# Optimization experiments

Measured on AMD Instinct MI355X. Metric: run time of the kernel, lower is better.

The kernel has to match this reference:

```python
import jax, jax.numpy as jnp
import numpy as np

B, S, DIM_IN, DIM_K, DIM_V = 8, 4096, 1024, 128, 128


def setup_inputs() -> dict:
    key = jax.random.key(0)
    ks = jax.random.split(key, 9)
    s_in = 1.0 / np.sqrt(DIM_IN)
    return {
        "query": jax.random.normal(ks[0], (B, S, DIM_IN), jnp.float32),
        "key": jax.random.normal(ks[1], (B, S, DIM_IN), jnp.float32),
        "value": jax.random.normal(ks[2], (B, S, DIM_IN), jnp.float32),
        # Linear params stored as [in, out] (torch weight transposed)
        "Wq": jax.random.uniform(ks[3], (DIM_IN, DIM_K), jnp.float32, -s_in, s_in),
        "bq": jax.random.uniform(ks[4], (DIM_K,), jnp.float32, -s_in, s_in),
        "Wk": jax.random.uniform(ks[5], (DIM_IN, DIM_K), jnp.float32, -s_in, s_in),
        "bk": jax.random.uniform(ks[6], (DIM_K,), jnp.float32, -s_in, s_in),
        "Wv": jax.random.uniform(ks[7], (DIM_IN, DIM_V), jnp.float32, -s_in, s_in),
        "bv": jax.random.uniform(ks[8], (DIM_V,), jnp.float32, -s_in, s_in),
    }


def reference(query, key, value, Wq, bq, Wk, bk, Wv, bv):
    q = jnp.einsum("bsd,dk->bsk", query, Wq) + bq   # [B,S,DIM_K]
    k = jnp.einsum("bsd,dk->bsk", key, Wk) + bk     # [B,S,DIM_K]
    v = jnp.einsum("bsd,dv->bsv", value, Wv) + bv   # [B,S,DIM_V]
    scale = 1.0 / jnp.sqrt(jnp.asarray(q.shape[-1], q.dtype))
    scores = jnp.einsum("bqk,bsk->bqs", q, k) * scale  # [B,S,S]
    attn = jax.nn.softmax(scores, axis=-1)
    return jnp.einsum("bqs,bsv->bqv", attn, v)  # [B,S,DIM_V]
```

## Files before the change

kernel.cpp:

```cpp
#include <hip/hip_runtime.h>
#include <hip/hip_bf16.h>

typedef __attribute__((ext_vector_type(8))) short short8;
typedef __attribute__((ext_vector_type(4))) float f32x4;
typedef __attribute__((ext_vector_type(16))) float f32x16;
typedef __attribute__((ext_vector_type(4))) unsigned int u32x4;

#define MFMA32(A, B, C) __builtin_amdgcn_mfma_f32_32x32x16_bf16((A), (B), (C), 0, 0, 0)

__device__ __forceinline__ short f2bf(float x) {
  unsigned u = __float_as_uint(x);
  return (short)((u + 0x7FFFu + ((u >> 16) & 1u)) >> 16);
}

__device__ __forceinline__ unsigned cvtpk(float lo, float hi) {
  unsigned r;
  asm("v_cvt_pk_bf16_f32 %0, %1, %2" : "=v"(r) : "v"(lo), "v"(hi));
  return r;
}

__device__ __forceinline__ void gload16(const void* g, const void* s) {
  __builtin_amdgcn_global_load_lds(
      (const __attribute__((address_space(1))) unsigned int*)g,
      (__attribute__((address_space(3))) unsigned int*)s, 16, 0, 0);
}

__global__ __launch_bounds__(256) void wt_kernel(
    const float* __restrict__ Wq, const float* __restrict__ Wk, const float* __restrict__ Wv,
    short* __restrict__ WqT, short* __restrict__ WkT, short* __restrict__ WvT)
{
  const float* W  = (blockIdx.y == 0) ? Wq  : (blockIdx.y == 1) ? Wk  : Wv;
  short*       WT = (blockIdx.y == 0) ? WqT : (blockIdx.y == 1) ? WkT : WvT;
  int idx = blockIdx.x * 256 + threadIdx.x;
  int n = idx >> 10, k = idx & 1023;
  WT[idx] = f2bf(W[k * 128 + n]);
}

__global__ __launch_bounds__(256, 2) void proj_kernel(
    const float* __restrict__ Aq, const float* __restrict__ Ak, const float* __restrict__ Av,
    const short* __restrict__ WqT, const short* __restrict__ WkT, const short* __restrict__ WvT,
    const float* __restrict__ bq, const float* __restrict__ bk, const float* __restrict__ bv,
    short* __restrict__ Qs, short* __restrict__ Ks, short* __restrict__ VTs,
    float scale_q)
{
  __shared__ short lds[32768];
  const int y = blockIdx.y;
  const float* A    = (y == 0) ? Aq  : (y == 1) ? Ak  : Av;
  const short* WT   = (y == 0) ? WqT : (y == 1) ? WkT : WvT;
  const float* bias = (y == 0) ? bq  : (y == 1) ? bk  : bv;
  const int tid = threadIdx.x, l = tid & 63, w = tid >> 6;
  const int l31 = l & 31, hi = l >> 5;
  const long m0 = (long)blockIdx.x * 128;
  const long mw = m0 + w * 32;

  const float* A0 = A + m0 * 1024;
  int ag[8];
  #pragma unroll
  for (int i = 0; i < 8; ++i) {
    int p = i * 4096 + tid * 16;
    int r_ = p >> 8;
    int c_ = (p & 255) ^ ((r_ & 15) << 4);
    ag[i] = r_ * 1024 + (c_ >> 2);
  }

  #define ASTAGE(bb, kc) { \
    const float* s_ = A0 + (kc) * 64; \
    _Pragma("unroll") \
    for (int i = 0; i < 8; ++i) \
      gload16(s_ + ag[i], &lds[(bb) * 16384 + i * 2048 + w * 512]); \
  }

  f32x16 acc0 = {}, acc1 = {}, acc2 = {}, acc3 = {};
  const char* abase = (const char*)lds;
  const int arow = w * 32 + l31;
  const int sw = (l31 & 15) << 4;
  const short* wl = WT + (long)l31 * 1024 + hi * 8;

  ASTAGE(0, 0);

  for (int kc = 0; kc < 16; ++kc) {
    const int bb = kc & 1;
    if (kc + 1 < 16) {
      ASTAGE(bb ^ 1, kc + 1);
      asm volatile("s_waitcnt vmcnt(8)" ::: "memory");
    } else {
      asm volatile("s_waitcnt vmcnt(0)" ::: "memory");
    }
    __builtin_amdgcn_s_barrier();

    const char* ab = abase + bb * 32768 + arow * 256;
    if (y < 2) {
      #pragma unroll
      for (int ks = 0; ks < 4; ++ks) {
        const int ac = ks * 64 + hi * 32;
        f32x4 a0 = *(const f32x4*)(ab + ((ac)      ^ sw));
        f32x4 a1 = *(const f32x4*)(ab + ((ac + 16) ^ sw));
        short8 af;
        af[0] = f2bf(a0[0]); af[1] = f2bf(a0[1]); af[2] = f2bf(a0[2]); af[3] = f2bf(a0[3]);
        af[4] = f2bf(a1[0]); af[5] = f2bf(a1[1]); af[6] = f2bf(a1[2]); af[7] = f2bf(a1[3]);
        const short* wp = wl + kc * 64 + ks * 16;
        short8 b0 = *(const short8*)(wp);
        short8 b1 = *(const short8*)(wp + 32768);
        short8 b2 = *(const short8*)(wp + 65536);
        short8 b3 = *(const short8*)(wp + 98304);
        acc0 = MFMA32(af, b0, acc0);
        acc1 = MFMA32(af, b1, acc1);
        acc2 = MFMA32(af, b2, acc2);
        acc3 = MFMA32(af, b3, acc3);
      }
    } else {
      #pragma unroll
      for (int ks = 0; ks < 4; ++ks) {
        const int ac = ks * 64 + hi * 32;
        f32x4 a0 = *(const f32x4*)(ab + ((ac)      ^ sw));
        f32x4 a1 = *(const f32x4*)(ab + ((ac + 16) ^ sw));
        short8 af;
        af[0] = f2bf(a0[0]); af[1] = f2bf(a0[1]); af[2] = f2bf(a0[2]); af[3] = f2bf(a0[3]);
        af[4] = f2bf(a1[0]); af[5] = f2bf(a1[1]); af[6] = f2bf(a1[2]); af[7] = f2bf(a1[3]);
        const short* wp = wl + kc * 64 + ks * 16;
        short8 b0 = *(const short8*)(wp);
        short8 b1 = *(const short8*)(wp + 32768);
        short8 b2 = *(const short8*)(wp + 65536);
        short8 b3 = *(const short8*)(wp + 98304);
        acc0 = MFMA32(b0, af, acc0);
        acc1 = MFMA32(b1, af, acc1);
        acc2 = MFMA32(b2, af, acc2);
        acc3 = MFMA32(b3, af, acc3);
      }
    }
    asm volatile("s_waitcnt lgkmcnt(0)" ::: "memory");
    __builtin_amdgcn_s_barrier();
  }

  if (y < 2) {
    short* Out = (y == 0) ? Qs : Ks;
    const float sc = (y == 0) ? scale_q : 1.0f;
#define PSTORE_QK(A_, nt) { \
    const int n_ = (nt) * 32 + l31; \
    const float bs_ = bias[n_]; \
    _Pragma("unroll") \
    for (int r = 0; r < 16; ++r) { \
      const int row_ = (r & 3) + 8 * (r >> 2) + 4 * hi; \
      Out[(mw + row_) * 128 + n_] = f2bf((A_[r] + bs_) * sc); \
    } }
    PSTORE_QK(acc0, 0) PSTORE_QK(acc1, 1) PSTORE_QK(acc2, 2) PSTORE_QK(acc3, 3)
  } else {
#define PSTORE_V(A_, nt) { \
    _Pragma("unroll") \
    for (int r = 0; r < 16; ++r) { \
      const int dv_ = (nt) * 32 + (r & 3) + 8 * (r >> 2) + 4 * hi; \
      VTs[(long)dv_ * 32768 + mw + l31] = f2bf(A_[r] + bias[dv_]); \
    } }
    PSTORE_V(acc0, 0) PSTORE_V(acc1, 1) PSTORE_V(acc2, 2) PSTORE_V(acc3, 3)
  }
}

__global__ __launch_bounds__(256, 2) void attn_kernel(
    const short* __restrict__ Q,
    const short* __restrict__ K,
    const short* __restrict__ VT,
    float* __restrict__ O0,
    float* __restrict__ O1,
    float2* __restrict__ stats,
    int ntiles)
{
  __shared__ short lds[32768];
  const int tid = threadIdx.x, l = tid & 63, w = tid >> 6;
  const int l31 = l & 31, hi = l >> 5, xm = (l & 7) << 3;
  const int qb = blockIdx.x, h = blockIdx.y;
  const int b = qb >> 5;
  const int qrow = qb * 128 + w * 32 + l31;
  const long kv0 = (long)b * 4096 + (long)h * ntiles * 64;

  short8 qf[8];
  const short* Qp = Q + (long)qrow * 128 + hi * 8;
  #pragma unroll
  for (int ds = 0; ds < 8; ++ds) qf[ds] = *(const short8*)(Qp + ds * 16);

  const short* Kt = K + kv0 * 128;
  const short* Vt = VT + kv0;
  int kg_off[4]; long vg_off[4];
  #pragma unroll
  for (int r = 0; r < 4; ++r) {
    int c = r * 256 + tid;
    int p = c * 16;
    kg_off[r] = (p ^ (((p >> 8) & 7) << 4)) >> 1;
    int e = (p ^ (((p >> 7) & 7) << 4)) >> 1;
    vg_off[r] = (long)(e >> 6) * 32768 + (e & 63);
  }

  #define STAGE(bb, t) { \
    const short* kg_ = Kt + (t) * 8192; \
    const short* vg_ = Vt + (t) * 64; \
    _Pragma("unroll") \
    for (int r = 0; r < 4; ++r) { \
      gload16(kg_ + kg_off[r], &lds[(bb) * 16384 + r * 2048 + w * 512]); \
      gload16(vg_ + vg_off[r], &lds[(bb) * 16384 + 8192 + r * 2048 + w * 512]); \
    } }

  f32x16 acc0 = {}, acc1 = {}, acc2 = {}, acc3 = {};
  float m = -3e38f, lsum = 0.f;
  const int kread = l31 * 128;

  STAGE(0, 0);

  for (int t = 0; t < ntiles; ++t) {
    const int bb = t & 1;
    if (t + 1 < ntiles) {
      STAGE(bb ^ 1, t + 1);
      asm volatile("s_waitcnt vmcnt(8)" ::: "memory");
    } else {
      asm volatile("s_waitcnt vmcnt(0)" ::: "memory");
    }
    __builtin_amdgcn_s_barrier();

    const short* kb = &lds[bb * 16384];
    const short* vb = &lds[bb * 16384 + 8192];

    f32x16 st0 = {}, st1 = {};
    #pragma unroll
    for (int ds = 0; ds < 8; ++ds) {
      int co = (ds * 16 + hi * 8) ^ xm;
      short8 kf0 = *(const short8*)(kb + kread + co);
      short8 kf1 = *(const short8*)(kb + 4096 + kread + co);
      st0 = MFMA32(kf0, qf[ds], st0);
      st1 = MFMA32(kf1, qf[ds], st1);
    }

    float a0 = fmaxf(fmaxf(st0[0], st0[1]),  fmaxf(st0[2], st0[3]));
    float a1 = fmaxf(fmaxf(st0[4], st0[5]),  fmaxf(st0[6], st0[7]));
    float a2 = fmaxf(fmaxf(st0[8], st0[9]),  fmaxf(st0[10], st0[11]));
    float a3 = fmaxf(fmaxf(st0[12], st0[13]), fmaxf(st0[14], st0[15]));
    float b0 = fmaxf(fmaxf(st1[0], st1[1]),  fmaxf(st1[2], st1[3]));
    float b1 = fmaxf(fmaxf(st1[4], st1[5]),  fmaxf(st1[6], st1[7]));
    float b2 = fmaxf(fmaxf(st1[8], st1[9]),  fmaxf(st1[10], st1[11]));
    float b3 = fmaxf(fmaxf(st1[12], st1[13]), fmaxf(st1[14], st1[15]));
    float pm = fmaxf(fmaxf(fmaxf(a0, a1), fmaxf(a2, a3)),
                     fmaxf(fmaxf(b0, b1), fmaxf(b2, b3)));
    pm = fmaxf(pm, __shfl_xor(pm, 32));
    if (!__all(pm <= m + 8.f)) {
      float mn = fmaxf(m, pm);
      float al = exp2f(m - mn);
      m = mn;
      lsum *= al;
      acc0 *= al; acc1 *= al; acc2 *= al; acc3 *= al;
    }
    float ts = 0.f;
    #pragma unroll
    for (int j = 0; j < 16; ++j) { st0[j] = exp2f(st0[j] - m); ts += st0[j]; }
    #pragma unroll
    for (int j = 0; j < 16; ++j) { st1[j] = exp2f(st1[j] - m); ts += st1[j]; }
    ts += __shfl_xor(ts, 32);
    lsum += ts;

    unsigned pk[16];
    #pragma unroll
    for (int j = 0; j < 8; ++j) pk[j]     = cvtpk(st0[2 * j], st0[2 * j + 1]);
    #pragma unroll
    for (int j = 0; j < 8; ++j) pk[8 + j] = cvtpk(st1[2 * j], st1[2 * j + 1]);

    #pragma unroll
    for (int f = 0; f < 4; ++f) {
      auto r02 = __builtin_amdgcn_permlane32_swap(pk[f * 4 + 0], pk[f * 4 + 2], false, false);
      auto r13 = __builtin_amdgcn_permlane32_swap(pk[f * 4 + 1], pk[f * 4 + 3], false, false);
      union { u32x4 u; short8 s; } pf;
      pf.u = (u32x4){r02[0], r13[0], r02[1], r13[1]};
      int vo = (f * 16 + hi * 8) ^ xm;
      acc0 = MFMA32(*(const short8*)(vb +        l31 * 64 + vo), pf.s, acc0);
      acc1 = MFMA32(*(const short8*)(vb + 2048 + l31 * 64 + vo), pf.s, acc1);
      acc2 = MFMA32(*(const short8*)(vb + 4096 + l31 * 64 + vo), pf.s, acc2);
      acc3 = MFMA32(*(const short8*)(vb + 6144 + l31 * 64 + vo), pf.s, acc3);
    }

    asm volatile("s_waitcnt lgkmcnt(0)" ::: "memory");
    __builtin_amdgcn_s_barrier();
  }

  float* Op = ((h == 0) ? O0 : O1) + (long)qrow * 128;
  #define STORE_DT(A, dtb) { \
    _Pragma("unroll") \
    for (int jj = 0; jj < 4; ++jj) { \
      f32x4 o_ = {A[4 * jj], A[4 * jj + 1], A[4 * jj + 2], A[4 * jj + 3]}; \
      *(f32x4*)(Op + (dtb) + jj * 8 + hi * 4) = o_; \
    } }
  STORE_DT(acc0, 0) STORE_DT(acc1, 32) STORE_DT(acc2, 64) STORE_DT(acc3, 96)

  if (l < 32) stats[(long)h * 32768 + qrow] = make_float2(m, lsum);
}

__global__ __launch_bounds__(256) void merge_kernel(
    float* __restrict__ O, const float* __restrict__ O1,
    const float2* __restrict__ stats, int halves)
{
  int idx = blockIdx.x * 256 + threadIdx.x;
  int q = idx >> 5, c = (idx & 31) * 4;
  long off = (long)q * 128 + c;
  float2 s0 = stats[q];
  f32x4 a = *(const f32x4*)(O + off);
  if (halves == 2) {
    float2 s1 = stats[32768 + q];
    float M = fmaxf(s0.x, s1.x);
    float w0 = exp2f(s0.x - M), w1 = exp2f(s1.x - M);
    f32x4 bv = *(const f32x4*)(O1 + off);
    float inv = 1.f / (w0 * s0.y + w1 * s1.y);
    a = (a * w0 + bv * w1) * inv;
  } else {
    a = a * (1.f / s0.y);
  }
  *(f32x4*)(O + off) = a;
}

extern "C" void kernel_launch(void* const* d_in, const int* in_sizes, int n_in,
                              void* d_out, int out_size, void* d_ws, size_t ws_size,
                              hipStream_t stream) {
  const float* query = (const float*)d_in[0];
  const float* key   = (const float*)d_in[1];
  const float* value = (const float*)d_in[2];
  const float* Wq = (const float*)d_in[3];
  const float* bq = (const float*)d_in[4];
  const float* Wk = (const float*)d_in[5];
  const float* bk = (const float*)d_in[6];
  const float* Wv = (const float*)d_in[7];
  const float* bv = (const float*)d_in[8];

  char* wsb = (char*)d_ws;
  short* Qs  = (short*)(wsb);
  short* Ks  = (short*)(wsb + 8388608);
  short* VTs = (short*)(wsb + 16777216);
  short* WqT = (short*)(wsb + 25165824);
  short* WkT = (short*)(wsb + 25427968);
  short* WvT = (short*)(wsb + 25690112);
  float* O1  = (float*)(wsb + 25952256);
  const size_t NEED2 = 25952256ull + 16777216ull + 524288ull;
  int halves = (ws_size >= NEED2) ? 2 : 1;
  float2* stats = (float2*)(wsb + (halves == 2 ? 42729472ull : 25952256ull));
  int ntiles = (halves == 2) ? 32 : 64;

  wt_kernel<<<dim3(512, 3), 256, 0, stream>>>(Wq, Wk, Wv, WqT, WkT, WvT);
  const float scale_q = 0.08838834764831845f * 1.4426950408889634f;
  proj_kernel<<<dim3(256, 3), 256, 0, stream>>>(query, key, value, WqT, WkT, WvT,
                                                bq, bk, bv, Qs, Ks, VTs, scale_q);
  attn_kernel<<<dim3(256, halves), 256, 0, stream>>>(Qs, Ks, VTs, (float*)d_out, O1, stats, ntiles);
  merge_kernel<<<4096, 256, 0, stream>>>((float*)d_out, O1, stats, halves);
}
```

Baseline: 244.5 us.

## Shrink projection tiles to 32 rows and split output columns across waves

The projection kernel now has each block handle 32 rows instead of 128, with each wave owning one 32-column slice of the output rather than its own 32 rows. K chunks grow to 256 floats, and the weight fragments are preloaded into registers per chunk. The grid is four times larger (1024x3 blocks), which raises parallelism and spreads the memory-bound activation stream across more CUs. The cost is that each block now reloads the full weight matrix from cache, and the 16-fragment preload adds register pressure.

```diff
diff --git a/kernel.cpp b/kernel.cpp
--- a/kernel.cpp
+++ b/kernel.cpp
@@ -43,44 +43,46 @@
     short* __restrict__ Qs, short* __restrict__ Ks, short* __restrict__ VTs,
     float scale_q)
 {
-  __shared__ short lds[32768];
+  __shared__ float lds[16384];
   const int y = blockIdx.y;
   const float* A    = (y == 0) ? Aq  : (y == 1) ? Ak  : Av;
   const short* WT   = (y == 0) ? WqT : (y == 1) ? WkT : WvT;
   const float* bias = (y == 0) ? bq  : (y == 1) ? bk  : bv;
   const int tid = threadIdx.x, l = tid & 63, w = tid >> 6;
   const int l31 = l & 31, hi = l >> 5;
-  const long m0 = (long)blockIdx.x * 128;
-  const long mw = m0 + w * 32;
+  const long m0 = (long)blockIdx.x * 32;
 
   const float* A0 = A + m0 * 1024;
   int ag[8];
   #pragma unroll
   for (int i = 0; i < 8; ++i) {
-    int p = i * 4096 + tid * 16;
-    int r_ = p >> 8;
-    int c_ = (p & 255) ^ ((r_ & 15) << 4);
-    ag[i] = r_ * 1024 + (c_ >> 2);
+    const int r_ = 8 * w + i;
+    const int cb = (l * 16) ^ ((r_ & 15) << 4);
+    ag[i] = r_ * 1024 + (cb >> 2);
   }
 
   #define ASTAGE(bb, kc) { \
-    const float* s_ = A0 + (kc) * 64; \
+    const float* s_ = A0 + (kc) * 256; \
     _Pragma("unroll") \
     for (int i = 0; i < 8; ++i) \
-      gload16(s_ + ag[i], &lds[(bb) * 16384 + i * 2048 + w * 512]); \
-  }
-
-  f32x16 acc0 = {}, acc1 = {}, acc2 = {}, acc3 = {};
+      gload16(s_ + ag[i], &lds[(bb) * 8192 + (8 * w + i) * 256]); \
+  }
+
+  f32x16 acc = {};
+  const int n_ = w * 32 + l31;
+  const short* Wn = WT + (long)n_ * 1024 + hi * 8;
   const char* abase = (const char*)lds;
-  const int arow = w * 32 + l31;
   const int sw = (l31 & 15) << 4;
-  const short* wl = WT + (long)l31 * 1024 + hi * 8;
 
   ASTAGE(0, 0);
 
-  for (int kc = 0; kc < 16; ++kc) {
+  for (int kc = 0; kc < 4; ++kc) {
     const int bb = kc & 1;
-    if (kc + 1 < 16) {
+    short8 wb[16];
+    #pragma unroll
+    for (int k16 = 0; k16 < 16; ++k16)
+      wb[k16] = *(const short8*)(Wn + kc * 256 + k16 * 16);
+    if (kc + 1 < 4) {
       ASTAGE(bb ^ 1, kc + 1);
       asm volatile("s_waitcnt vmcnt(8)" ::: "memory");
     } else {
@@ -88,44 +90,28 @@
     }
     __builtin_amdgcn_s_barrier();
 
-    const char* ab = abase + bb * 32768 + arow * 256;
+    const char* ab = abase + bb * 32768 + l31 * 1024;
     if (y < 2) {
       #pragma unroll
-      for (int ks = 0; ks < 4; ++ks) {
-        const int ac = ks * 64 + hi * 32;
-        f32x4 a0 = *(const f32x4*)(ab + ((ac)      ^ sw));
-        f32x4 a1 = *(const f32x4*)(ab + ((ac + 16) ^ sw));
+      for (int k16 = 0; k16 < 16; ++k16) {
+        const int c = k16 * 64 + hi * 32;
+        f32x4 a0 = *(const f32x4*)(ab + ((c)      ^ sw));
+        f32x4 a1 = *(const f32x4*)(ab + ((c + 16) ^ sw));
         short8 af;
         af[0] = f2bf(a0[0]); af[1] = f2bf(a0[1]); af[2] = f2bf(a0[2]); af[3] = f2bf(a0[3]);
         af[4] = f2bf(a1[0]); af[5] = f2bf(a1[1]); af[6] = f2bf(a1[2]); af[7] = f2bf(a1[3]);
-        const short* wp = wl + kc * 64 + ks * 16;
-        short8 b0 = *(const short8*)(wp);
-        short8 b1 = *(const short8*)(wp + 32768);
-        short8 b2 = *(const short8*)(wp + 65536);
-        short8 b3 = *(const short8*)(wp + 98304);
-        acc0 = MFMA32(af, b0, acc0);
-        acc1 = MFMA32(af, b1, acc1);
-        acc2 = MFMA32(af, b2, acc2);
-        acc3 = MFMA32(af, b3, acc3);
+        acc = MFMA32(af, wb[k16], acc);
       }
     } else {
       #pragma unroll
-      for (int ks = 0; ks < 4; ++ks) {
-        const int ac = ks * 64 + hi * 32;
-        f32x4 a0 = *(const f32x4*)(ab + ((ac)      ^ sw));
-        f32x4 a1 = *(const f32x4*)(ab + ((ac + 16) ^ sw));
+      for (int k16 = 0; k16 < 16; ++k16) {
+        const int c = k16 * 64 + hi * 32;
+        f32x4 a0 = *(const f32x4*)(ab + ((c)      ^ sw));
+        f32x4 a1 = *(const f32x4*)(ab + ((c + 16) ^ sw));
         short8 af;
         af[0] = f2bf(a0[0]); af[1] = f2bf(a0[1]); af[2] = f2bf(a0[2]); af[3] = f2bf(a0[3]);
         af[4] = f2bf(a1[0]); af[5] = f2bf(a1[1]); af[6] = f2bf(a1[2]); af[7] = f2bf(a1[3]);
-        const short* wp = wl + kc * 64 + ks * 16;
-        short8 b0 = *(const short8*)(wp);
-        short8 b1 = *(const short8*)(wp + 32768);
-        short8 b2 = *(const short8*)(wp + 65536);
-        short8 b3 = *(const short8*)(wp + 98304);
-        acc0 = MFMA32(b0, af, acc0);
-        acc1 = MFMA32(b1, af, acc1);
-        acc2 = MFMA32(b2, af, acc2);
-        acc3 = MFMA32(b3, af, acc3);
+        acc = MFMA32(wb[k16], af, acc);
       }
     }
     asm volatile("s_waitcnt lgkmcnt(0)" ::: "memory");
@@ -135,23 +121,18 @@
   if (y < 2) {
     short* Out = (y == 0) ? Qs : Ks;
     const float sc = (y == 0) ? scale_q : 1.0f;
-#define PSTORE_QK(A_, nt) { \
-    const int n_ = (nt) * 32 + l31; \
-    const float bs_ = bias[n_]; \
-    _Pragma("unroll") \
-    for (int r = 0; r < 16; ++r) { \
-      const int row_ = (r & 3) + 8 * (r >> 2) + 4 * hi; \
-      Out[(mw + row_) * 128 + n_] = f2bf((A_[r] + bs_) * sc); \
-    } }
-    PSTORE_QK(acc0, 0) PSTORE_QK(acc1, 1) PSTORE_QK(acc2, 2) PSTORE_QK(acc3, 3)
+    const float bs = bias[n_];
+    #pragma unroll
+    for (int r = 0; r < 16; ++r) {
+      const int row_ = (r & 3) + 8 * (r >> 2) + 4 * hi;
+      Out[(m0 + row_) * 128 + n_] = f2bf((acc[r] + bs) * sc);
+    }
   } else {
-#define PSTORE_V(A_, nt) { \
-    _Pragma("unroll") \
-    for (int r = 0; r < 16; ++r) { \
-      const int dv_ = (nt) * 32 + (r & 3) + 8 * (r >> 2) + 4 * hi; \
-      VTs[(long)dv_ * 32768 + mw + l31] = f2bf(A_[r] + bias[dv_]); \
-    } }
-    PSTORE_V(acc0, 0) PSTORE_V(acc1, 1) PSTORE_V(acc2, 2) PSTORE_V(acc3, 3)
+    #pragma unroll
+    for (int r = 0; r < 16; ++r) {
+      const int dv_ = w * 32 + (r & 3) + 8 * (r >> 2) + 4 * hi;
+      VTs[(long)dv_ * 32768 + m0 + l31] = f2bf(acc[r] + bias[dv_]);
+    }
   }
 }
 
@@ -338,8 +319,8 @@
 
   wt_kernel<<<dim3(512, 3), 256, 0, stream>>>(Wq, Wk, Wv, WqT, WkT, WvT);
   const float scale_q = 0.08838834764831845f * 1.4426950408889634f;
-  proj_kernel<<<dim3(256, 3), 256, 0, stream>>>(query, key, value, WqT, WkT, WvT,
-                                                bq, bk, bv, Qs, Ks, VTs, scale_q);
+  proj_kernel<<<dim3(1024, 3), 256, 0, stream>>>(query, key, value, WqT, WkT, WvT,
+                                                 bq, bk, bv, Qs, Ks, VTs, scale_q);
   attn_kernel<<<dim3(256, halves), 256, 0, stream>>>(Qs, Ks, VTs, (float*)d_out, O1, stats, ntiles);
   merge_kernel<<<4096, 256, 0, stream>>>((float*)d_out, O1, stats, halves);
 }
```

Result: no change. 248.0 us (+1.4%).
